# Optimization experiments

Measured on AMD Instinct MI355X. Metric: run time of the kernel, lower is better.

## Reference

```python
import jax, jax.numpy as jnp
import numpy as np

N_NODES = 100000
N_EDGES = 1600000
HIDDEN = 128
N_CLASSES = 40
# torch.rand(1).item() in apply_randalign; fixed here for a deterministic reference
ALPHA = 0.62


def setup_inputs() -> dict:
    key = jax.random.key(0)
    ks = jax.random.split(key, 6)
    inputs = jax.random.normal(ks[0], (N_NODES, HIDDEN), jnp.float32)
    src = jax.random.randint(ks[1], (N_EDGES,), 0, N_NODES, jnp.int32)
    dst = jax.random.randint(ks[2], (N_EDGES,), 0, N_NODES, jnp.int32)
    s = 1.0 / np.sqrt(HIDDEN)
    W1 = jax.random.normal(ks[3], (HIDDEN, HIDDEN), jnp.float32) * s
    W2 = jax.random.normal(ks[4], (HIDDEN, HIDDEN), jnp.float32) * s
    W3 = jax.random.normal(ks[5], (HIDDEN, N_CLASSES), jnp.float32) * s
    return dict(inputs=inputs, src=src, dst=dst,
                W1=W1, b1=jnp.zeros((HIDDEN,), jnp.float32),
                W2=W2, b2=jnp.zeros((HIDDEN,), jnp.float32),
                W3=W3, b3=jnp.zeros((N_CLASSES,), jnp.float32))


def _graph_conv(x, W, b, src, dst):
    # DGL GraphConv, norm='both': D_dst^{-1/2} A D_src^{-1/2} X W + b
    n = x.shape[0]
    ones = jnp.ones(src.shape, x.dtype)
    deg_out = jnp.clip(jax.ops.segment_sum(ones, src, num_segments=n), 1.0)
    deg_in = jnp.clip(jax.ops.segment_sum(ones, dst, num_segments=n), 1.0)
    h = (x @ W) * (deg_out ** -0.5)[:, None]          # row scaling commutes with XW
    agg = jax.ops.segment_sum(h[src], dst, num_segments=n)
    return agg * (deg_in ** -0.5)[:, None] + b


def _randalign(h_prev, h_curr, alpha):
    norm_prev = jnp.linalg.norm(h_prev, axis=1, keepdims=True)
    norm_curr = jnp.linalg.norm(h_curr, axis=1, keepdims=True)
    scaled_prev = h_prev * (norm_curr / norm_prev)
    return alpha * h_curr + (1.0 - alpha) * scaled_prev


def reference(inputs, src, dst, W1, b1, W2, b2, W3, b3):
    # Faithful to source: layers[0] is never applied; loop runs over layers[1..-2].
    h = jax.nn.relu(_graph_conv(inputs, W1, b1, src, dst))      # i = 1
    h_next = jax.nn.relu(_graph_conv(h, W2, b2, src, dst))      # i = 2
    h = _randalign(h, h_next, ALPHA)
    logits = _graph_conv(h, W3, b3, src, dst)                   # final layer
    return logits
```

## Files before the change

### kernel.cpp

```cpp
#include <hip/hip_runtime.h>
#include <hip/hip_bf16.h>

#define HIDDEN 128
#define ALPHA_F 0.62f
#define CAP 64
#define BKT_BITS 9
#define BCAP 10240
#define CSTRIDE 132

typedef __attribute__((ext_vector_type(8))) short bf16x8;
typedef __attribute__((ext_vector_type(4))) float f32x4;

__device__ inline unsigned short f2bf(float f) {
  unsigned u = __float_as_uint(f);
  unsigned r = (u + 0x7fffu + ((u >> 16) & 1u)) >> 16;
  return (unsigned short)r;
}
__device__ inline float bf2f(unsigned short h) {
  return __uint_as_float((unsigned)h << 16);
}

__device__ inline f32x4 mfma_bf16(bf16x8 a, bf16x8 b, f32x4 c) {
  return __builtin_amdgcn_mfma_f32_16x16x32_bf16(a, b, c, 0, 0, 0);
}

template <int CT, bool OUTBF16>
__device__ void gemm_mfma_body(const float* __restrict__ A,
                               const unsigned short* __restrict__ WhT,
                               const unsigned short* __restrict__ WlT,
                               void* __restrict__ outp, int n, int NW, int gi,
                               unsigned* __restrict__ smem) {
  unsigned short* s16 = (unsigned short*)smem;
  const int t = threadIdx.x;
  const int wv = t >> 6, l = t & 63;
  const int lr = l & 15, lg = (l >> 4) & 3;
  const int rb = gi * 128;

  constexpr int WSLOTS = 4 * CT * 64;
  for (int s = t; s < WSLOTS; s += 256) {
    int sl = s & 63;
    int cc = s >> 6;
    int ct = cc % CT, c = cc / CT;
    int col = ct * 16 + (sl & 15);
    int k = c * 32 + ((sl >> 4) & 3) * 8;
    uint4 hv = *(const uint4*)&WhT[(size_t)col * HIDDEN + k];
    uint4 lv = *(const uint4*)&WlT[(size_t)col * HIDDEN + k];
    *(uint4*)&s16[(cc * 2 + 0) * 512 + sl * 8] = hv;
    *(uint4*)&s16[(cc * 2 + 1) * 512 + sl * 8] = lv;
  }

  f32x4 acc[2][CT];
#pragma unroll
  for (int rt = 0; rt < 2; rt++)
#pragma unroll
    for (int ct = 0; ct < CT; ct++)
#pragma unroll
      for (int e = 0; e < 4; e++) acc[rt][ct][e] = 0.f;

  __syncthreads();

  for (int c = 0; c < 4; c++) {
    bf16x8 ah[2], al[2];
#pragma unroll
    for (int rt = 0; rt < 2; rt++) {
      int rr = rb + wv * 32 + rt * 16 + lr;
      if (rr >= n) rr = n - 1;
      const float4* g = (const float4*)(A + (size_t)rr * HIDDEN + c * 32 + lg * 8);
      float4 v0 = g[0], v1 = g[1];
      float f[8] = {v0.x, v0.y, v0.z, v0.w, v1.x, v1.y, v1.z, v1.w};
#pragma unroll
      for (int q = 0; q < 8; q++) {
        unsigned short h = f2bf(f[q]);
        ah[rt][q] = (short)h;
        al[rt][q] = (short)f2bf(f[q] - bf2f(h));
      }
    }
#pragma unroll
    for (int ct = 0; ct < CT; ct++) {
      int cc = c * CT + ct;
      bf16x8 bh = *(const bf16x8*)&s16[(cc * 2 + 0) * 512 + l * 8];
      bf16x8 bl = *(const bf16x8*)&s16[(cc * 2 + 1) * 512 + l * 8];
#pragma unroll
      for (int rt = 0; rt < 2; rt++) {
        acc[rt][ct] = mfma_bf16(ah[rt], bh, acc[rt][ct]);
        acc[rt][ct] = mfma_bf16(al[rt], bh, acc[rt][ct]);
        acc[rt][ct] = mfma_bf16(ah[rt], bl, acc[rt][ct]);
      }
    }
  }

  if (OUTBF16) {
    __syncthreads();
    unsigned short* cr = s16 + wv * (32 * CSTRIDE);
    int lg4 = lg;
#pragma unroll
    for (int rt = 0; rt < 2; rt++)
#pragma unroll
      for (int ct = 0; ct < CT; ct++)
#pragma unroll
        for (int r = 0; r < 4; r++)
          cr[(rt * 16 + lg4 * 4 + r) * CSTRIDE + ct * 16 + lr] = f2bf(acc[rt][ct][r]);
#pragma unroll
    for (int ps = 0; ps < 8; ps++) {
      int row_local = ps * 4 + lg4;
      int orow = rb + wv * 32 + row_local;
      if (orow < n) {
        uint4 v = *(const uint4*)&cr[row_local * CSTRIDE + lr * 8];
        *(uint4*)&((unsigned short*)outp)[(size_t)orow * NW + lr * 8] = v;
      }
    }
  } else {
#pragma unroll
    for (int rt = 0; rt < 2; rt++) {
#pragma unroll
      for (int ct = 0; ct < CT; ct++) {
#pragma unroll
        for (int r = 0; r < 4; r++) {
          int orow = rb + wv * 32 + rt * 16 + lg * 4 + r;
          int ocol = ct * 16 + lr;
          if (orow < n && ocol < NW)
            ((float*)outp)[(size_t)orow * NW + ocol] = acc[rt][ct][r];
        }
      }
    }
  }
}

__global__ __launch_bounds__(256) void partition_kernel(
    const int* __restrict__ src, const int* __restrict__ dst, int E, int nbkt,
    unsigned* __restrict__ gcur1, unsigned* __restrict__ gcur2,
    unsigned* __restrict__ stg1, unsigned short* __restrict__ stg2, int pa_blocks,
    const float* __restrict__ W1, const float* __restrict__ W2, const float* __restrict__ W3,
    unsigned short* __restrict__ W1h, unsigned short* __restrict__ W1l,
    unsigned short* __restrict__ W2h, unsigned short* __restrict__ W2l,
    unsigned short* __restrict__ W3h, unsigned short* __restrict__ W3l, int NC) {
  const int t = threadIdx.x;
  const int bid = blockIdx.x;
  if (bid >= pa_blocks) {
    int r = bid - pa_blocks;
    const float* W = (r == 0) ? W1 : (r == 1) ? W2 : W3;
    unsigned short* Wh = (r == 0) ? W1h : (r == 1) ? W2h : W3h;
    unsigned short* Wl = (r == 0) ? W1l : (r == 1) ? W2l : W3l;
    int ncol = (r == 2) ? 48 : 128;
    int nw   = (r == 2) ? NC : 128;
    for (int idx = t; idx < ncol * HIDDEN; idx += 256) {
      int c = idx >> 7, k = idx & 127;
      float v = (c < nw) ? W[(size_t)k * nw + c] : 0.f;
      unsigned short hi = f2bf(v);
      Wh[idx] = hi;
      Wl[idx] = f2bf(v - bf2f(hi));
    }
    return;
  }
  __shared__ unsigned h1[256], h2[256], b1[256], b2[256];
  h1[t] = 0; h2[t] = 0;
  __syncthreads();
  const int chunk = (E + pa_blocks - 1) / pa_blocks;
  const int e0 = bid * chunk, e1 = min(e0 + chunk, E);
  for (int e = e0 + t; e < e1; e += 256) {
    atomicAdd(&h1[(unsigned)dst[e] >> BKT_BITS], 1u);
    atomicAdd(&h2[(unsigned)src[e] >> BKT_BITS], 1u);
  }
  __syncthreads();
  if (t < nbkt) {
    b1[t] = atomicAdd(&gcur1[t], h1[t]);
    b2[t] = atomicAdd(&gcur2[t], h2[t]);
  }
  h1[t] = 0; h2[t] = 0;
  __syncthreads();
  for (int e = e0 + t; e < e1; e += 256) {
    int s = src[e], d = dst[e];
    unsigned bk1 = (unsigned)d >> BKT_BITS;
    unsigned p1 = b1[bk1] + atomicAdd(&h1[bk1], 1u);
    if (p1 < BCAP) stg1[(size_t)bk1 * BCAP + p1] = ((unsigned)s << BKT_BITS) | ((unsigned)d & 511u);
    unsigned bk2 = (unsigned)s >> BKT_BITS;
    unsigned p2 = b2[bk2] + atomicAdd(&h2[bk2], 1u);
    if (p2 < BCAP) stg2[(size_t)bk2 * BCAP + p2] = (unsigned short)(s & 511);
  }
}

__global__ __launch_bounds__(256) void csr_and_gemm1_kernel(
    const unsigned* __restrict__ gcur1, const unsigned* __restrict__ gcur2,
    const unsigned* __restrict__ stg1, const unsigned short* __restrict__ stg2,
    int* __restrict__ csr, int* __restrict__ deg_in, int* __restrict__ deg_out,
    int n, int nbkt,
    const float* __restrict__ X,
    const unsigned short* __restrict__ W1h, const unsigned short* __restrict__ W1l,
    unsigned short* __restrict__ T1) {
  __shared__ __align__(16) unsigned smem[16384];
  const int bid = blockIdx.x;
  if (bid >= 2 * nbkt) {
    gemm_mfma_body<8, true>(X, W1h, W1l, T1, n, HIDDEN, bid - 2 * nbkt, smem);
    return;
  }
  int* cnt = (int*)smem;
  const int t = threadIdx.x;
  cnt[t] = 0; cnt[t + 256] = 0;
  __syncthreads();
  if (bid < nbkt) {
    const int b = bid;
    const int m = min((int)gcur1[b], BCAP);
    const int node0 = b << BKT_BITS;
    for (int i = t; i < m; i += 256) {
      unsigned val = stg1[(size_t)b * BCAP + i];
      int dl = val & 511;
      int s = (int)(val >> BKT_BITS);
      int pos = atomicAdd(&cnt[dl], 1);
      if (pos < CAP) csr[((size_t)(node0 + dl) << 6) + pos] = s;
    }
    __syncthreads();
    for (int u = t; u < 512; u += 256) {
      int node = node0 + u;
      if (node < n) deg_in[node] = cnt[u];
    }
  } else {
    const int b = bid - nbkt;
    const int m = min((int)gcur2[b], BCAP);
    const int node0 = b << BKT_BITS;
    for (int i = t; i < m; i += 256) {
      atomicAdd(&cnt[stg2[(size_t)b * BCAP + i]], 1);
    }
    __syncthreads();
    for (int u = t; u < 512; u += 256) {
      int node = node0 + u;
      if (node < n) deg_out[node] = cnt[u];
    }
  }
}

__global__ __launch_bounds__(256) void gemm2_kernel(
    const float* __restrict__ A,
    const unsigned short* __restrict__ Wh, const unsigned short* __restrict__ Wl,
    unsigned short* __restrict__ T, int n) {
  __shared__ __align__(16) unsigned smem[16384];
  gemm_mfma_body<8, true>(A, Wh, Wl, T, n, HIDDEN, blockIdx.x, smem);
}

__global__ __launch_bounds__(256) void gemm3_kernel(
    const float* __restrict__ A,
    const unsigned short* __restrict__ Wh, const unsigned short* __restrict__ Wl,
    float* __restrict__ T, int n, int NW) {
  __shared__ __align__(16) unsigned smem[6144];
  gemm_mfma_body<3, false>(A, Wh, Wl, T, n, NW, blockIdx.x, smem);
}

template <bool RA>
__global__ __launch_bounds__(128) void gather_bf16_kernel(
    const unsigned* __restrict__ Tu, const int* __restrict__ csr,
    const int* __restrict__ deg_out, const int* __restrict__ deg_in,
    const float* __restrict__ bias, const float* __restrict__ Hprev,
    float* __restrict__ out, int n) {
  const int w = threadIdx.x >> 6;
  const int lane = threadIdx.x & 63;
  const int v = blockIdx.x * 2 + w;
  if (v >= n) return;
  __shared__ int s_idx[2][64];
  __shared__ float s_w[2][64];
  const int deg = deg_in[v];
  const int m = min(deg, CAP);
  int u0 = (lane < m) ? csr[((size_t)v << 6) + lane] : 0;
  s_idx[w][lane] = u0;
  s_w[w][lane] = (lane < m) ? rsqrtf((float)max(deg_out[u0], 1)) : 0.f;

  float a0 = 0.f, a1 = 0.f, b0 = 0.f, b1 = 0.f, c0 = 0.f, c1 = 0.f, d0 = 0.f, d1 = 0.f;
  int j = 0;
  for (; j + 4 <= m; j += 4) {
    unsigned x0 = Tu[((size_t)s_idx[w][j] << 6) + lane];
    unsigned x1 = Tu[((size_t)s_idx[w][j + 1] << 6) + lane];
    unsigned x2 = Tu[((size_t)s_idx[w][j + 2] << 6) + lane];
    unsigned x3 = Tu[((size_t)s_idx[w][j + 3] << 6) + lane];
    float w0 = s_w[w][j], w1 = s_w[w][j + 1], w2 = s_w[w][j + 2], w3 = s_w[w][j + 3];
    a0 = fmaf(w0, __uint_as_float(x0 << 16), a0);
    a1 = fmaf(w0, __uint_as_float(x0 & 0xffff0000u), a1);
    b0 = fmaf(w1, __uint_as_float(x1 << 16), b0);
    b1 = fmaf(w1, __uint_as_float(x1 & 0xffff0000u), b1);
    c0 = fmaf(w2, __uint_as_float(x2 << 16), c0);
    c1 = fmaf(w2, __uint_as_float(x2 & 0xffff0000u), c1);
    d0 = fmaf(w3, __uint_as_float(x3 << 16), d0);
    d1 = fmaf(w3, __uint_as_float(x3 & 0xffff0000u), d1);
  }
  for (; j < m; j++) {
    unsigned x0 = Tu[((size_t)s_idx[w][j] << 6) + lane];
    float w0 = s_w[w][j];
    a0 = fmaf(w0, __uint_as_float(x0 << 16), a0);
    a1 = fmaf(w0, __uint_as_float(x0 & 0xffff0000u), a1);
  }
  float slo = (a0 + b0) + (c0 + d0);
  float shi = (a1 + b1) + (c1 + d1);
  float din = rsqrtf((float)max(deg, 1));
  float2 bias2 = ((const float2*)bias)[lane];
  float r0 = fmaxf(slo * din + bias2.x, 0.f);
  float r1 = fmaxf(shi * din + bias2.y, 0.f);
  if (RA) {
    float2 p = ((const float2*)(Hprev + (size_t)v * HIDDEN))[lane];
    float sc = r0 * r0 + r1 * r1;
    float sp = p.x * p.x + p.y * p.y;
#pragma unroll
    for (int off = 1; off < 64; off <<= 1) {
      sc += __shfl_xor(sc, off);
      sp += __shfl_xor(sp, off);
    }
    float ratio = sqrtf(sc) / sqrtf(sp);
    r0 = ALPHA_F * r0 + (1.0f - ALPHA_F) * p.x * ratio;
    r1 = ALPHA_F * r1 + (1.0f - ALPHA_F) * p.y * ratio;
  }
  ((float2*)(out + (size_t)v * HIDDEN))[lane] = make_float2(r0, r1);
}

__global__ __launch_bounds__(128) void gather_f32_kernel(
    const float* __restrict__ T3, const int* __restrict__ csr,
    const int* __restrict__ deg_out, const int* __restrict__ deg_in,
    const float* __restrict__ bias, float* __restrict__ out, int n, int NC) {
  const int w = threadIdx.x >> 6;
  const int lane = threadIdx.x & 63;
  const int v = blockIdx.x * 2 + w;
  if (v >= n) return;
  __shared__ int s_idx[2][64];
  __shared__ float s_w[2][64];
  const int deg = deg_in[v];
  const int m = min(deg, CAP);
  int u0 = (lane < m) ? csr[((size_t)v << 6) + lane] : 0;
  s_idx[w][lane] = u0;
  s_w[w][lane] = (lane < m) ? rsqrtf((float)max(deg_out[u0], 1)) : 0.f;

  float a0 = 0.f, a1 = 0.f, a2 = 0.f, a3 = 0.f;
  if (lane < NC) {
    int j = 0;
    for (; j + 4 <= m; j += 4) {
      a0 = fmaf(s_w[w][j],     T3[(size_t)s_idx[w][j] * NC + lane], a0);
      a1 = fmaf(s_w[w][j + 1], T3[(size_t)s_idx[w][j + 1] * NC + lane], a1);
      a2 = fmaf(s_w[w][j + 2], T3[(size_t)s_idx[w][j + 2] * NC + lane], a2);
      a3 = fmaf(s_w[w][j + 3], T3[(size_t)s_idx[w][j + 3] * NC + lane], a3);
    }
    for (; j < m; j++) a0 = fmaf(s_w[w][j], T3[(size_t)s_idx[w][j] * NC + lane], a0);
    float din = rsqrtf((float)max(deg, 1));
    out[(size_t)v * NC + lane] = ((a0 + a1) + (a2 + a3)) * din + bias[lane];
  }
}

extern "C" void kernel_launch(void* const* d_in, const int* in_sizes, int n_in,
                              void* d_out, int out_size, void* d_ws, size_t ws_size,
                              hipStream_t stream) {
  const float* X  = (const float*)d_in[0];
  const int* src  = (const int*)d_in[1];
  const int* dst  = (const int*)d_in[2];
  const float* W1 = (const float*)d_in[3];
  const float* b1 = (const float*)d_in[4];
  const float* W2 = (const float*)d_in[5];
  const float* b2 = (const float*)d_in[6];
  const float* W3 = (const float*)d_in[7];
  const float* b3 = (const float*)d_in[8];
  float* out = (float*)d_out;

  const int n = in_sizes[0] / HIDDEN;
  const int E = in_sizes[1];
  const int NC = in_sizes[8];
  const int nbkt = (n + 511) >> BKT_BITS;

  char* p = (char*)d_ws;
  auto alloc = [&](size_t bytes) {
    char* r = p;
    p += (bytes + 255) & ~(size_t)255;
    return r;
  };
  unsigned* gcur1 = (unsigned*)alloc(512 * 4);
  unsigned* gcur2 = gcur1 + 256;
  int* deg_out    = (int*)alloc((size_t)n * 4);
  int* deg_in     = (int*)alloc((size_t)n * 4);
  int* csr        = (int*)alloc((size_t)n * CAP * 4);
  unsigned short* stg2 = (unsigned short*)alloc((size_t)256 * BCAP * 2);
  unsigned* stg1  = (unsigned*)alloc((size_t)256 * BCAP * 4);
  unsigned short* BufT = (unsigned short*)alloc((size_t)n * HIDDEN * 2);
  float* BufB     = (float*)alloc((size_t)n * HIDDEN * 4);
  unsigned short* W1h = (unsigned short*)alloc(128 * 128 * 2);
  unsigned short* W1l = (unsigned short*)alloc(128 * 128 * 2);
  unsigned short* W2h = (unsigned short*)alloc(128 * 128 * 2);
  unsigned short* W2l = (unsigned short*)alloc(128 * 128 * 2);
  unsigned short* W3h = (unsigned short*)alloc(48 * 128 * 2);
  unsigned short* W3l = (unsigned short*)alloc(48 * 128 * 2);

  hipMemsetAsync(gcur1, 0, 512 * 4, stream);

  const int PA = 256;
  partition_kernel<<<PA + 3, 256, 0, stream>>>(src, dst, E, nbkt, gcur1, gcur2, stg1, stg2, PA,
                                               W1, W2, W3, W1h, W1l, W2h, W2l, W3h, W3l, NC);

  int gb = (n + 127) / 128;
  csr_and_gemm1_kernel<<<2 * nbkt + gb, 256, 0, stream>>>(gcur1, gcur2, stg1, stg2,
                                                          csr, deg_in, deg_out, n, nbkt,
                                                          X, W1h, W1l, BufT);
  int hb = (n + 1) / 2;
  gather_bf16_kernel<false><<<hb, 128, 0, stream>>>((const unsigned*)BufT, csr, deg_out, deg_in, b1, nullptr, BufB, n);
  gemm2_kernel<<<gb, 256, 0, stream>>>(BufB, W2h, W2l, BufT, n);
  gather_bf16_kernel<true><<<hb, 128, 0, stream>>>((const unsigned*)BufT, csr, deg_out, deg_in, b2, BufB, BufB, n);
  gemm3_kernel<<<gb, 256, 0, stream>>>(BufB, W3h, W3l, (float*)BufT, n, NC);
  gather_f32_kernel<<<hb, 128, 0, stream>>>((const float*)BufT, csr, deg_out, deg_in, b3, out, n, NC);
}
```

Baseline: 329.1 us.

## Fuse neighbor gather with following GEMM and store layer-3 features as bf16

Merges each aggregation kernel with the next layer's MFMA GEMM: a 512-thread block gathers 128 node rows into swizzled shared memory as split hi/lo bf16, then multiplies them by the weights, which are read directly from global memory. This removes the fp32 round trip of the hidden activations for layer 2 and of the aligned activations before layer 3, and removes two launches. The layer-3 projection is padded to 64 columns and stored as bf16 instead of fp32, so the final gather reads half as many bytes but with lower precision. Neighbor indices move from shared memory to wave shuffles, and gathering 16 nodes serially per wave may reduce latency hiding.

```diff
diff --git a/kernel.cpp b/kernel.cpp
--- a/kernel.cpp
+++ b/kernel.cpp
@@ -6,7 +6,7 @@
 #define CAP 64
 #define BKT_BITS 9
 #define BCAP 10240
-#define CSTRIDE 132
+#define CSTRIDE 136
 
 typedef __attribute__((ext_vector_type(8))) short bf16x8;
 typedef __attribute__((ext_vector_type(4))) float f32x4;
@@ -24,11 +24,11 @@
   return __builtin_amdgcn_mfma_f32_16x16x32_bf16(a, b, c, 0, 0, 0);
 }
 
-template <int CT, bool OUTBF16>
+template <int CT>
 __device__ void gemm_mfma_body(const float* __restrict__ A,
                                const unsigned short* __restrict__ WhT,
                                const unsigned short* __restrict__ WlT,
-                               void* __restrict__ outp, int n, int NW, int gi,
+                               unsigned short* __restrict__ outp, int n, int NW, int gi,
                                unsigned* __restrict__ smem) {
   unsigned short* s16 = (unsigned short*)smem;
   const int t = threadIdx.x;
@@ -89,39 +89,22 @@
     }
   }
 
-  if (OUTBF16) {
-    __syncthreads();
-    unsigned short* cr = s16 + wv * (32 * CSTRIDE);
-    int lg4 = lg;
-#pragma unroll
-    for (int rt = 0; rt < 2; rt++)
-#pragma unroll
-      for (int ct = 0; ct < CT; ct++)
-#pragma unroll
-        for (int r = 0; r < 4; r++)
-          cr[(rt * 16 + lg4 * 4 + r) * CSTRIDE + ct * 16 + lr] = f2bf(acc[rt][ct][r]);
-#pragma unroll
-    for (int ps = 0; ps < 8; ps++) {
-      int row_local = ps * 4 + lg4;
-      int orow = rb + wv * 32 + row_local;
-      if (orow < n) {
-        uint4 v = *(const uint4*)&cr[row_local * CSTRIDE + lr * 8];
-        *(uint4*)&((unsigned short*)outp)[(size_t)orow * NW + lr * 8] = v;
-      }
-    }
-  } else {
-#pragma unroll
-    for (int rt = 0; rt < 2; rt++) {
-#pragma unroll
-      for (int ct = 0; ct < CT; ct++) {
-#pragma unroll
-        for (int r = 0; r < 4; r++) {
-          int orow = rb + wv * 32 + rt * 16 + lg * 4 + r;
-          int ocol = ct * 16 + lr;
-          if (orow < n && ocol < NW)
-            ((float*)outp)[(size_t)orow * NW + ocol] = acc[rt][ct][r];
-        }
-      }
+  __syncthreads();
+  unsigned short* cr = s16 + wv * (32 * CSTRIDE);
+#pragma unroll
+  for (int rt = 0; rt < 2; rt++)
+#pragma unroll
+    for (int ct = 0; ct < CT; ct++)
+#pragma unroll
+      for (int r = 0; r < 4; r++)
+        cr[(rt * 16 + lg * 4 + r) * CSTRIDE + ct * 16 + lr] = f2bf(acc[rt][ct][r]);
+#pragma unroll
+  for (int ps = 0; ps < 8; ps++) {
+    int row_local = ps * 4 + lg;
+    int orow = rb + wv * 32 + row_local;
+    if (orow < n) {
+      uint4 v = *(const uint4*)&cr[row_local * CSTRIDE + lr * 8];
+      *(uint4*)&outp[(size_t)orow * NW + lr * 8] = v;
     }
   }
 }
@@ -141,7 +124,7 @@
     const float* W = (r == 0) ? W1 : (r == 1) ? W2 : W3;
     unsigned short* Wh = (r == 0) ? W1h : (r == 1) ? W2h : W3h;
     unsigned short* Wl = (r == 0) ? W1l : (r == 1) ? W2l : W3l;
-    int ncol = (r == 2) ? 48 : 128;
+    int ncol = (r == 2) ? 64 : 128;
     int nw   = (r == 2) ? NC : 128;
     for (int idx = t; idx < ncol * HIDDEN; idx += 256) {
       int c = idx >> 7, k = idx & 127;
@@ -190,7 +173,7 @@
   __shared__ __align__(16) unsigned smem[16384];
   const int bid = blockIdx.x;
   if (bid >= 2 * nbkt) {
-    gemm_mfma_body<8, true>(X, W1h, W1l, T1, n, HIDDEN, bid - 2 * nbkt, smem);
+    gemm_mfma_body<8>(X, W1h, W1l, T1, n, HIDDEN, bid - 2 * nbkt, smem);
     return;
   }
   int* cnt = (int*)smem;
@@ -228,113 +211,171 @@
   }
 }
 
-__global__ __launch_bounds__(256) void gemm2_kernel(
-    const float* __restrict__ A,
-    const unsigned short* __restrict__ Wh, const unsigned short* __restrict__ Wl,
-    unsigned short* __restrict__ T, int n) {
-  __shared__ __align__(16) unsigned smem[16384];
-  gemm_mfma_body<8, true>(A, Wh, Wl, T, n, HIDDEN, blockIdx.x, smem);
-}
-
-__global__ __launch_bounds__(256) void gemm3_kernel(
-    const float* __restrict__ A,
-    const unsigned short* __restrict__ Wh, const unsigned short* __restrict__ Wl,
-    float* __restrict__ T, int n, int NW) {
-  __shared__ __align__(16) unsigned smem[6144];
-  gemm_mfma_body<3, false>(A, Wh, Wl, T, n, NW, blockIdx.x, smem);
-}
-
-template <bool RA>
-__global__ __launch_bounds__(128) void gather_bf16_kernel(
+template <int CT, bool RAB>
+__global__ __launch_bounds__(512) void fused_gather_gemm_kernel(
     const unsigned* __restrict__ Tu, const int* __restrict__ csr,
     const int* __restrict__ deg_out, const int* __restrict__ deg_in,
-    const float* __restrict__ bias, const float* __restrict__ Hprev,
-    float* __restrict__ out, int n) {
-  const int w = threadIdx.x >> 6;
-  const int lane = threadIdx.x & 63;
-  const int v = blockIdx.x * 2 + w;
+    const float* __restrict__ bias, float* __restrict__ Hglob,
+    const unsigned short* __restrict__ WhT, const unsigned short* __restrict__ WlT,
+    unsigned short* __restrict__ outT, int n) {
+  __shared__ __align__(16) unsigned short sH[2][128 * 128];
+  const int t = threadIdx.x;
+  const int wv = t >> 6, l = t & 63;
+  const int lr = l & 15, lg = (l >> 4) & 3;
+  const int rb = blockIdx.x * 128;
+
+  for (int nl = 0; nl < 16; nl++) {
+    const int r = wv * 16 + nl;
+    const int v = rb + r;
+    float r0 = 0.f, r1 = 0.f;
+    if (v < n) {
+      const int deg = deg_in[v];
+      const int m = min(deg, CAP);
+      int iu = (l < m) ? csr[((size_t)v << 6) + l] : 0;
+      float wu = (l < m) ? rsqrtf((float)max(deg_out[iu], 1)) : 0.f;
+      float a0 = 0.f, a1 = 0.f, b0 = 0.f, b1 = 0.f, c0 = 0.f, c1 = 0.f, d0 = 0.f, d1 = 0.f;
+      int j = 0;
+      for (; j + 4 <= m; j += 4) {
+        int u0 = __shfl(iu, j), u1 = __shfl(iu, j + 1), u2 = __shfl(iu, j + 2), u3 = __shfl(iu, j + 3);
+        float w0 = __shfl(wu, j), w1 = __shfl(wu, j + 1), w2 = __shfl(wu, j + 2), w3 = __shfl(wu, j + 3);
+        unsigned x0 = Tu[((size_t)u0 << 6) + l];
+        unsigned x1 = Tu[((size_t)u1 << 6) + l];
+        unsigned x2 = Tu[((size_t)u2 << 6) + l];
+        unsigned x3 = Tu[((size_t)u3 << 6) + l];
+        a0 = fmaf(w0, __uint_as_float(x0 << 16), a0);
+        a1 = fmaf(w0, __uint_as_float(x0 & 0xffff0000u), a1);
+        b0 = fmaf(w1, __uint_as_float(x1 << 16), b0);
+        b1 = fmaf(w1, __uint_as_float(x1 & 0xffff0000u), b1);
+        c0 = fmaf(w2, __uint_as_float(x2 << 16), c0);
+        c1 = fmaf(w2, __uint_as_float(x2 & 0xffff0000u), c1);
+        d0 = fmaf(w3, __uint_as_float(x3 << 16), d0);
+        d1 = fmaf(w3, __uint_as_float(x3 & 0xffff0000u), d1);
+      }
+      for (; j < m; j++) {
+        int u0 = __shfl(iu, j);
+        float w0 = __shfl(wu, j);
+        unsigned x0 = Tu[((size_t)u0 << 6) + l];
+        a0 = fmaf(w0, __uint_as_float(x0 << 16), a0);
+        a1 = fmaf(w0, __uint_as_float(x0 & 0xffff0000u), a1);
+      }
+      float slo = (a0 + b0) + (c0 + d0);
+      float shi = (a1 + b1) + (c1 + d1);
+      float din = rsqrtf((float)max(deg, 1));
+      float2 bias2 = ((const float2*)bias)[l];
+      r0 = fmaxf(slo * din + bias2.x, 0.f);
+      r1 = fmaxf(shi * din + bias2.y, 0.f);
+      if (!RAB) {
+        ((float2*)(Hglob + (size_t)v * HIDDEN))[l] = make_float2(r0, r1);
+      } else {
+        float2 pp = ((const float2*)(Hglob + (size_t)v * HIDDEN))[l];
+        float sc = r0 * r0 + r1 * r1;
+        float sp = pp.x * pp.x + pp.y * pp.y;
+#pragma unroll
+        for (int off = 1; off < 64; off <<= 1) {
+          sc += __shfl_xor(sc, off);
+          sp += __shfl_xor(sp, off);
+        }
+        float ratio = sqrtf(sc) / sqrtf(sp);
+        r0 = ALPHA_F * r0 + (1.0f - ALPHA_F) * pp.x * ratio;
+        r1 = ALPHA_F * r1 + (1.0f - ALPHA_F) * pp.y * ratio;
+      }
+    }
+    int off16 = r * 128 + (((l >> 2) ^ (r & 15)) << 3) + ((2 * l) & 7);
+    unsigned short h0 = f2bf(r0), h1v = f2bf(r1);
+    unsigned short q0 = f2bf(r0 - bf2f(h0)), q1 = f2bf(r1 - bf2f(h1v));
+    *(unsigned*)&sH[0][off16] = (unsigned)h0 | ((unsigned)h1v << 16);
+    *(unsigned*)&sH[1][off16] = (unsigned)q0 | ((unsigned)q1 << 16);
+  }
+
+  f32x4 acc[CT];
+#pragma unroll
+  for (int ct = 0; ct < CT; ct++)
+#pragma unroll
+    for (int e = 0; e < 4; e++) acc[ct][e] = 0.f;
+
+  const int ar = wv * 16 + lr;
+  for (int c = 0; c < 4; c++) {
+    int bidx = ((c * 4 + lg) ^ (ar & 15)) << 3;
+    bf16x8 ah = *(const bf16x8*)&sH[0][ar * 128 + bidx];
+    bf16x8 al = *(const bf16x8*)&sH[1][ar * 128 + bidx];
+#pragma unroll
+    for (int ct = 0; ct < CT; ct++) {
+      int col = ct * 16 + lr;
+      bf16x8 bh = *(const bf16x8*)&WhT[(size_t)col * HIDDEN + c * 32 + lg * 8];
+      bf16x8 bl = *(const bf16x8*)&WlT[(size_t)col * HIDDEN + c * 32 + lg * 8];
+      acc[ct] = mfma_bf16(ah, bh, acc[ct]);
+      acc[ct] = mfma_bf16(al, bh, acc[ct]);
+      acc[ct] = mfma_bf16(ah, bl, acc[ct]);
+    }
+  }
+
+  __syncthreads();
+  unsigned short* cr = &sH[0][0] + wv * (16 * CSTRIDE);
+#pragma unroll
+  for (int ct = 0; ct < CT; ct++)
+#pragma unroll
+    for (int r = 0; r < 4; r++)
+      cr[(lg * 4 + r) * CSTRIDE + ct * 16 + lr] = f2bf(acc[ct][r]);
+  constexpr int NW = CT * 16;
+#pragma unroll
+  for (int ps = 0; ps < 4; ps++) {
+    int row_local = ps * 4 + lg;
+    int orow = rb + wv * 16 + row_local;
+    if (orow < n && lr * 8 < NW) {
+      uint4 v = *(const uint4*)&cr[row_local * CSTRIDE + lr * 8];
+      *(uint4*)&outT[(size_t)orow * NW + lr * 8] = v;
+    }
+  }
+}
+
+__global__ __launch_bounds__(256) void gather_final_kernel(
+    const unsigned* __restrict__ Tu3, const int* __restrict__ csr,
+    const int* __restrict__ deg_out, const int* __restrict__ deg_in,
+    const float* __restrict__ bias, float* __restrict__ out, int n, int NC) {
+  const int wv = threadIdx.x >> 6, l = threadIdx.x & 63;
+  const int v = blockIdx.x * 4 + wv;
   if (v >= n) return;
-  __shared__ int s_idx[2][64];
-  __shared__ float s_w[2][64];
   const int deg = deg_in[v];
   const int m = min(deg, CAP);
-  int u0 = (lane < m) ? csr[((size_t)v << 6) + lane] : 0;
-  s_idx[w][lane] = u0;
-  s_w[w][lane] = (lane < m) ? rsqrtf((float)max(deg_out[u0], 1)) : 0.f;
-
+  int iu = (l < m) ? csr[((size_t)v << 6) + l] : 0;
+  float wu = (l < m) ? rsqrtf((float)max(deg_out[iu], 1)) : 0.f;
   float a0 = 0.f, a1 = 0.f, b0 = 0.f, b1 = 0.f, c0 = 0.f, c1 = 0.f, d0 = 0.f, d1 = 0.f;
+  const bool act = (l < 20);
   int j = 0;
   for (; j + 4 <= m; j += 4) {
-    unsigned x0 = Tu[((size_t)s_idx[w][j] << 6) + lane];
-    unsigned x1 = Tu[((size_t)s_idx[w][j + 1] << 6) + lane];
-    unsigned x2 = Tu[((size_t)s_idx[w][j + 2] << 6) + lane];
-    unsigned x3 = Tu[((size_t)s_idx[w][j + 3] << 6) + lane];
-    float w0 = s_w[w][j], w1 = s_w[w][j + 1], w2 = s_w[w][j + 2], w3 = s_w[w][j + 3];
-    a0 = fmaf(w0, __uint_as_float(x0 << 16), a0);
-    a1 = fmaf(w0, __uint_as_float(x0 & 0xffff0000u), a1);
-    b0 = fmaf(w1, __uint_as_float(x1 << 16), b0);
-    b1 = fmaf(w1, __uint_as_float(x1 & 0xffff0000u), b1);
-    c0 = fmaf(w2, __uint_as_float(x2 << 16), c0);
-    c1 = fmaf(w2, __uint_as_float(x2 & 0xffff0000u), c1);
-    d0 = fmaf(w3, __uint_as_float(x3 << 16), d0);
-    d1 = fmaf(w3, __uint_as_float(x3 & 0xffff0000u), d1);
+    int u0 = __shfl(iu, j), u1 = __shfl(iu, j + 1), u2 = __shfl(iu, j + 2), u3 = __shfl(iu, j + 3);
+    float w0 = __shfl(wu, j), w1 = __shfl(wu, j + 1), w2 = __shfl(wu, j + 2), w3 = __shfl(wu, j + 3);
+    if (act) {
+      unsigned x0 = Tu3[((size_t)u0 << 5) + l];
+      unsigned x1 = Tu3[((size_t)u1 << 5) + l];
+      unsigned x2 = Tu3[((size_t)u2 << 5) + l];
+      unsigned x3 = Tu3[((size_t)u3 << 5) + l];
+      a0 = fmaf(w0, __uint_as_float(x0 << 16), a0);
+      a1 = fmaf(w0, __uint_as_float(x0 & 0xffff0000u), a1);
+      b0 = fmaf(w1, __uint_as_float(x1 << 16), b0);
+      b1 = fmaf(w1, __uint_as_float(x1 & 0xffff0000u), b1);
+      c0 = fmaf(w2, __uint_as_float(x2 << 16), c0);
+      c1 = fmaf(w2, __uint_as_float(x2 & 0xffff0000u), c1);
+      d0 = fmaf(w3, __uint_as_float(x3 << 16), d0);
+      d1 = fmaf(w3, __uint_as_float(x3 & 0xffff0000u), d1);
+    }
   }
   for (; j < m; j++) {
-    unsigned x0 = Tu[((size_t)s_idx[w][j] << 6) + lane];
-    float w0 = s_w[w][j];
-    a0 = fmaf(w0, __uint_as_float(x0 << 16), a0);
-    a1 = fmaf(w0, __uint_as_float(x0 & 0xffff0000u), a1);
-  }
-  float slo = (a0 + b0) + (c0 + d0);
-  float shi = (a1 + b1) + (c1 + d1);
-  float din = rsqrtf((float)max(deg, 1));
-  float2 bias2 = ((const float2*)bias)[lane];
-  float r0 = fmaxf(slo * din + bias2.x, 0.f);
-  float r1 = fmaxf(shi * din + bias2.y, 0.f);
-  if (RA) {
-    float2 p = ((const float2*)(Hprev + (size_t)v * HIDDEN))[lane];
-    float sc = r0 * r0 + r1 * r1;
-    float sp = p.x * p.x + p.y * p.y;
-#pragma unroll
-    for (int off = 1; off < 64; off <<= 1) {
-      sc += __shfl_xor(sc, off);
-      sp += __shfl_xor(sp, off);
-    }
-    float ratio = sqrtf(sc) / sqrtf(sp);
-    r0 = ALPHA_F * r0 + (1.0f - ALPHA_F) * p.x * ratio;
-    r1 = ALPHA_F * r1 + (1.0f - ALPHA_F) * p.y * ratio;
-  }
-  ((float2*)(out + (size_t)v * HIDDEN))[lane] = make_float2(r0, r1);
-}
-
-__global__ __launch_bounds__(128) void gather_f32_kernel(
-    const float* __restrict__ T3, const int* __restrict__ csr,
-    const int* __restrict__ deg_out, const int* __restrict__ deg_in,
-    const float* __restrict__ bias, float* __restrict__ out, int n, int NC) {
-  const int w = threadIdx.x >> 6;
-  const int lane = threadIdx.x & 63;
-  const int v = blockIdx.x * 2 + w;
-  if (v >= n) return;
-  __shared__ int s_idx[2][64];
-  __shared__ float s_w[2][64];
-  const int deg = deg_in[v];
-  const int m = min(deg, CAP);
-  int u0 = (lane < m) ? csr[((size_t)v << 6) + lane] : 0;
-  s_idx[w][lane] = u0;
-  s_w[w][lane] = (lane < m) ? rsqrtf((float)max(deg_out[u0], 1)) : 0.f;
-
-  float a0 = 0.f, a1 = 0.f, a2 = 0.f, a3 = 0.f;
-  if (lane < NC) {
-    int j = 0;
-    for (; j + 4 <= m; j += 4) {
-      a0 = fmaf(s_w[w][j],     T3[(size_t)s_idx[w][j] * NC + lane], a0);
-      a1 = fmaf(s_w[w][j + 1], T3[(size_t)s_idx[w][j + 1] * NC + lane], a1);
-      a2 = fmaf(s_w[w][j + 2], T3[(size_t)s_idx[w][j + 2] * NC + lane], a2);
-      a3 = fmaf(s_w[w][j + 3], T3[(size_t)s_idx[w][j + 3] * NC + lane], a3);
-    }
-    for (; j < m; j++) a0 = fmaf(s_w[w][j], T3[(size_t)s_idx[w][j] * NC + lane], a0);
+    int u0 = __shfl(iu, j);
+    float w0 = __shfl(wu, j);
+    if (act) {
+      unsigned x0 = Tu3[((size_t)u0 << 5) + l];
+      a0 = fmaf(w0, __uint_as_float(x0 << 16), a0);
+      a1 = fmaf(w0, __uint_as_float(x0 & 0xffff0000u), a1);
+    }
+  }
+  if (act) {
+    float slo = (a0 + b0) + (c0 + d0);
+    float shi = (a1 + b1) + (c1 + d1);
     float din = rsqrtf((float)max(deg, 1));
-    out[(size_t)v * NC + lane] = ((a0 + a1) + (a2 + a3)) * din + bias[lane];
+    float2 bias2 = ((const float2*)bias)[l];
+    float2 o = make_float2(slo * din + bias2.x, shi * din + bias2.y);
+    *(float2*)(out + (size_t)v * NC + 2 * l) = o;
   }
 }
 
@@ -370,14 +411,15 @@
   int* csr        = (int*)alloc((size_t)n * CAP * 4);
   unsigned short* stg2 = (unsigned short*)alloc((size_t)256 * BCAP * 2);
   unsigned* stg1  = (unsigned*)alloc((size_t)256 * BCAP * 4);
-  unsigned short* BufT = (unsigned short*)alloc((size_t)n * HIDDEN * 2);
+  unsigned short* BufT1 = (unsigned short*)alloc((size_t)n * HIDDEN * 2);
+  unsigned short* BufT2 = (unsigned short*)alloc((size_t)n * HIDDEN * 2);
   float* BufB     = (float*)alloc((size_t)n * HIDDEN * 4);
   unsigned short* W1h = (unsigned short*)alloc(128 * 128 * 2);
   unsigned short* W1l = (unsigned short*)alloc(128 * 128 * 2);
   unsigned short* W2h = (unsigned short*)alloc(128 * 128 * 2);
   unsigned short* W2l = (unsigned short*)alloc(128 * 128 * 2);
-  unsigned short* W3h = (unsigned short*)alloc(48 * 128 * 2);
-  unsigned short* W3l = (unsigned short*)alloc(48 * 128 * 2);
+  unsigned short* W3h = (unsigned short*)alloc(64 * 128 * 2);
+  unsigned short* W3l = (unsigned short*)alloc(64 * 128 * 2);
 
   hipMemsetAsync(gcur1, 0, 512 * 4, stream);
 
@@ -388,11 +430,11 @@
   int gb = (n + 127) / 128;
   csr_and_gemm1_kernel<<<2 * nbkt + gb, 256, 0, stream>>>(gcur1, gcur2, stg1, stg2,
                                                           csr, deg_in, deg_out, n, nbkt,
-                                                          X, W1h, W1l, BufT);
-  int hb = (n + 1) / 2;
-  gather_bf16_kernel<false><<<hb, 128, 0, stream>>>((const unsigned*)BufT, csr, deg_out, deg_in, b1, nullptr, BufB, n);
-  gemm2_kernel<<<gb, 256, 0, stream>>>(BufB, W2h, W2l, BufT, n);
-  gather_bf16_kernel<true><<<hb, 128, 0, stream>>>((const unsigned*)BufT, csr, deg_out, deg_in, b2, BufB, BufB, n);
-  gemm3_kernel<<<gb, 256, 0, stream>>>(BufB, W3h, W3l, (float*)BufT, n, NC);
-  gather_f32_kernel<<<hb, 128, 0, stream>>>((const float*)BufT, csr, deg_out, deg_in, b3, out, n, NC);
-}
+                                                          X, W1h, W1l, BufT1);
+  fused_gather_gemm_kernel<8, false><<<gb, 512, 0, stream>>>(
+      (const unsigned*)BufT1, csr, deg_out, deg_in, b1, BufB, W2h, W2l, BufT2, n);
+  fused_gather_gemm_kernel<4, true><<<gb, 512, 0, stream>>>(
+      (const unsigned*)BufT2, csr, deg_out, deg_in, b2, BufB, W3h, W3l, BufT1, n);
+  gather_final_kernel<<<(n + 3) / 4, 256, 0, stream>>>(
+      (const unsigned*)BufT1, csr, deg_out, deg_in, b3, out, n, NC);
+}
```

Result: slower. 453.0 us (+37.7%).

## Widen gather loads, store layer-3 projection as bf16, process several edges per wave

Applied to the files above, without the earlier changes.

The gather kernels now have each lane load 8 bytes (4 bf16 features), so a single wave handles two neighbors at once (or four in the final layer). Neighbor indices and weights move through wave shuffles instead of shared memory, and the halves are summed with cross-lane reductions. The third GEMM now pads to 64 columns and writes bf16 through the shared-memory staging path, which halves the bytes gathered in the final layer. Blocks grow to 4 waves each. The cost is lower precision in the final-layer intermediate and some extra shuffle work.

```diff
diff --git a/kernel.cpp b/kernel.cpp
--- a/kernel.cpp
+++ b/kernel.cpp
@@ -6,7 +6,7 @@
 #define CAP 64
 #define BKT_BITS 9
 #define BCAP 10240
-#define CSTRIDE 132
+#define CSTRIDE 136
 
 typedef __attribute__((ext_vector_type(8))) short bf16x8;
 typedef __attribute__((ext_vector_type(4))) float f32x4;
@@ -19,16 +19,18 @@
 __device__ inline float bf2f(unsigned short h) {
   return __uint_as_float((unsigned)h << 16);
 }
+__device__ inline float bflo(unsigned x) { return __uint_as_float(x << 16); }
+__device__ inline float bfhi(unsigned x) { return __uint_as_float(x & 0xffff0000u); }
 
 __device__ inline f32x4 mfma_bf16(bf16x8 a, bf16x8 b, f32x4 c) {
   return __builtin_amdgcn_mfma_f32_16x16x32_bf16(a, b, c, 0, 0, 0);
 }
 
-template <int CT, bool OUTBF16>
+template <int CT>
 __device__ void gemm_mfma_body(const float* __restrict__ A,
                                const unsigned short* __restrict__ WhT,
                                const unsigned short* __restrict__ WlT,
-                               void* __restrict__ outp, int n, int NW, int gi,
+                               unsigned short* __restrict__ outp, int n, int NW, int gi,
                                unsigned* __restrict__ smem) {
   unsigned short* s16 = (unsigned short*)smem;
   const int t = threadIdx.x;
@@ -89,39 +91,22 @@
     }
   }
 
-  if (OUTBF16) {
-    __syncthreads();
-    unsigned short* cr = s16 + wv * (32 * CSTRIDE);
-    int lg4 = lg;
-#pragma unroll
-    for (int rt = 0; rt < 2; rt++)
-#pragma unroll
-      for (int ct = 0; ct < CT; ct++)
-#pragma unroll
-        for (int r = 0; r < 4; r++)
-          cr[(rt * 16 + lg4 * 4 + r) * CSTRIDE + ct * 16 + lr] = f2bf(acc[rt][ct][r]);
-#pragma unroll
-    for (int ps = 0; ps < 8; ps++) {
-      int row_local = ps * 4 + lg4;
-      int orow = rb + wv * 32 + row_local;
-      if (orow < n) {
-        uint4 v = *(const uint4*)&cr[row_local * CSTRIDE + lr * 8];
-        *(uint4*)&((unsigned short*)outp)[(size_t)orow * NW + lr * 8] = v;
-      }
-    }
-  } else {
-#pragma unroll
-    for (int rt = 0; rt < 2; rt++) {
-#pragma unroll
-      for (int ct = 0; ct < CT; ct++) {
-#pragma unroll
-        for (int r = 0; r < 4; r++) {
-          int orow = rb + wv * 32 + rt * 16 + lg * 4 + r;
-          int ocol = ct * 16 + lr;
-          if (orow < n && ocol < NW)
-            ((float*)outp)[(size_t)orow * NW + ocol] = acc[rt][ct][r];
-        }
-      }
+  __syncthreads();
+  unsigned short* cr = s16 + wv * (32 * CSTRIDE);
+#pragma unroll
+  for (int rt = 0; rt < 2; rt++)
+#pragma unroll
+    for (int ct = 0; ct < CT; ct++)
+#pragma unroll
+      for (int r = 0; r < 4; r++)
+        cr[(rt * 16 + lg * 4 + r) * CSTRIDE + ct * 16 + lr] = f2bf(acc[rt][ct][r]);
+#pragma unroll
+  for (int ps = 0; ps < 8; ps++) {
+    int row_local = ps * 4 + lg;
+    int orow = rb + wv * 32 + row_local;
+    if (orow < n && lr * 8 < NW) {
+      uint4 v = *(const uint4*)&cr[row_local * CSTRIDE + lr * 8];
+      *(uint4*)&outp[(size_t)orow * NW + lr * 8] = v;
     }
   }
 }
@@ -141,7 +126,7 @@
     const float* W = (r == 0) ? W1 : (r == 1) ? W2 : W3;
     unsigned short* Wh = (r == 0) ? W1h : (r == 1) ? W2h : W3h;
     unsigned short* Wl = (r == 0) ? W1l : (r == 1) ? W2l : W3l;
-    int ncol = (r == 2) ? 48 : 128;
+    int ncol = (r == 2) ? 64 : 128;
     int nw   = (r == 2) ? NC : 128;
     for (int idx = t; idx < ncol * HIDDEN; idx += 256) {
       int c = idx >> 7, k = idx & 127;
@@ -190,7 +175,7 @@
   __shared__ __align__(16) unsigned smem[16384];
   const int bid = blockIdx.x;
   if (bid >= 2 * nbkt) {
-    gemm_mfma_body<8, true>(X, W1h, W1l, T1, n, HIDDEN, bid - 2 * nbkt, smem);
+    gemm_mfma_body<8>(X, W1h, W1l, T1, n, HIDDEN, bid - 2 * nbkt, smem);
     return;
   }
   int* cnt = (int*)smem;
@@ -233,108 +218,119 @@
     const unsigned short* __restrict__ Wh, const unsigned short* __restrict__ Wl,
     unsigned short* __restrict__ T, int n) {
   __shared__ __align__(16) unsigned smem[16384];
-  gemm_mfma_body<8, true>(A, Wh, Wl, T, n, HIDDEN, blockIdx.x, smem);
+  gemm_mfma_body<8>(A, Wh, Wl, T, n, HIDDEN, blockIdx.x, smem);
 }
 
 __global__ __launch_bounds__(256) void gemm3_kernel(
     const float* __restrict__ A,
     const unsigned short* __restrict__ Wh, const unsigned short* __restrict__ Wl,
-    float* __restrict__ T, int n, int NW) {
-  __shared__ __align__(16) unsigned smem[6144];
-  gemm_mfma_body<3, false>(A, Wh, Wl, T, n, NW, blockIdx.x, smem);
+    unsigned short* __restrict__ T, int n) {
+  __shared__ __align__(16) unsigned smem[9000];
+  gemm_mfma_body<4>(A, Wh, Wl, T, n, 64, blockIdx.x, smem);
 }
 
 template <bool RA>
-__global__ __launch_bounds__(128) void gather_bf16_kernel(
+__global__ __launch_bounds__(256) void gather_conv_kernel(
     const unsigned* __restrict__ Tu, const int* __restrict__ csr,
     const int* __restrict__ deg_out, const int* __restrict__ deg_in,
-    const float* __restrict__ bias, const float* __restrict__ Hprev,
-    float* __restrict__ out, int n) {
-  const int w = threadIdx.x >> 6;
-  const int lane = threadIdx.x & 63;
-  const int v = blockIdx.x * 2 + w;
+    const float* __restrict__ bias, float* __restrict__ H, int n) {
+  const int wv = threadIdx.x >> 6, l = threadIdx.x & 63;
+  const int v = blockIdx.x * 4 + wv;
   if (v >= n) return;
-  __shared__ int s_idx[2][64];
-  __shared__ float s_w[2][64];
+  const int half = l >> 5, cg = l & 31;
   const int deg = deg_in[v];
   const int m = min(deg, CAP);
-  int u0 = (lane < m) ? csr[((size_t)v << 6) + lane] : 0;
-  s_idx[w][lane] = u0;
-  s_w[w][lane] = (lane < m) ? rsqrtf((float)max(deg_out[u0], 1)) : 0.f;
-
-  float a0 = 0.f, a1 = 0.f, b0 = 0.f, b1 = 0.f, c0 = 0.f, c1 = 0.f, d0 = 0.f, d1 = 0.f;
+  int iu = (l < m) ? csr[((size_t)v << 6) + l] : 0;
+  float wu = (l < m) ? rsqrtf((float)max(deg_out[iu], 1)) : 0.f;
+
+  const uint2* Tr = (const uint2*)Tu;
+  float a0 = 0.f, a1 = 0.f, a2 = 0.f, a3 = 0.f;
+  float b0 = 0.f, b1 = 0.f, b2 = 0.f, b3 = 0.f;
   int j = 0;
-  for (; j + 4 <= m; j += 4) {
-    unsigned x0 = Tu[((size_t)s_idx[w][j] << 6) + lane];
-    unsigned x1 = Tu[((size_t)s_idx[w][j + 1] << 6) + lane];
-    unsigned x2 = Tu[((size_t)s_idx[w][j + 2] << 6) + lane];
-    unsigned x3 = Tu[((size_t)s_idx[w][j + 3] << 6) + lane];
-    float w0 = s_w[w][j], w1 = s_w[w][j + 1], w2 = s_w[w][j + 2], w3 = s_w[w][j + 3];
-    a0 = fmaf(w0, __uint_as_float(x0 << 16), a0);
-    a1 = fmaf(w0, __uint_as_float(x0 & 0xffff0000u), a1);
-    b0 = fmaf(w1, __uint_as_float(x1 << 16), b0);
-    b1 = fmaf(w1, __uint_as_float(x1 & 0xffff0000u), b1);
-    c0 = fmaf(w2, __uint_as_float(x2 << 16), c0);
-    c1 = fmaf(w2, __uint_as_float(x2 & 0xffff0000u), c1);
-    d0 = fmaf(w3, __uint_as_float(x3 << 16), d0);
-    d1 = fmaf(w3, __uint_as_float(x3 & 0xffff0000u), d1);
-  }
-  for (; j < m; j++) {
-    unsigned x0 = Tu[((size_t)s_idx[w][j] << 6) + lane];
-    float w0 = s_w[w][j];
-    a0 = fmaf(w0, __uint_as_float(x0 << 16), a0);
-    a1 = fmaf(w0, __uint_as_float(x0 & 0xffff0000u), a1);
-  }
-  float slo = (a0 + b0) + (c0 + d0);
-  float shi = (a1 + b1) + (c1 + d1);
+  for (; j + 2 < m; j += 4) {
+    int eA = j + half, eB = j + 2 + half;
+    int uA = __shfl(iu, eA), uB = __shfl(iu, eB);
+    float wA = __shfl(wu, eA), wB = __shfl(wu, eB);
+    uint2 xA = Tr[(size_t)uA * 32 + cg];
+    uint2 xB = Tr[(size_t)uB * 32 + cg];
+    a0 = fmaf(wA, bflo(xA.x), a0); a1 = fmaf(wA, bfhi(xA.x), a1);
+    a2 = fmaf(wA, bflo(xA.y), a2); a3 = fmaf(wA, bfhi(xA.y), a3);
+    b0 = fmaf(wB, bflo(xB.x), b0); b1 = fmaf(wB, bfhi(xB.x), b1);
+    b2 = fmaf(wB, bflo(xB.y), b2); b3 = fmaf(wB, bfhi(xB.y), b3);
+  }
+  for (; j < m; j += 2) {
+    int eA = j + half;
+    int uA = __shfl(iu, eA);
+    float wA = __shfl(wu, eA);
+    uint2 xA = Tr[(size_t)uA * 32 + cg];
+    a0 = fmaf(wA, bflo(xA.x), a0); a1 = fmaf(wA, bfhi(xA.x), a1);
+    a2 = fmaf(wA, bflo(xA.y), a2); a3 = fmaf(wA, bfhi(xA.y), a3);
+  }
+  a0 += b0; a1 += b1; a2 += b2; a3 += b3;
+  a0 += __shfl_xor(a0, 32);
+  a1 += __shfl_xor(a1, 32);
+  a2 += __shfl_xor(a2, 32);
+  a3 += __shfl_xor(a3, 32);
+
   float din = rsqrtf((float)max(deg, 1));
-  float2 bias2 = ((const float2*)bias)[lane];
-  float r0 = fmaxf(slo * din + bias2.x, 0.f);
-  float r1 = fmaxf(shi * din + bias2.y, 0.f);
+  float4 bias4 = ((const float4*)bias)[cg];
+  float r0 = fmaxf(a0 * din + bias4.x, 0.f);
+  float r1 = fmaxf(a1 * din + bias4.y, 0.f);
+  float r2 = fmaxf(a2 * din + bias4.z, 0.f);
+  float r3 = fmaxf(a3 * din + bias4.w, 0.f);
+
   if (RA) {
-    float2 p = ((const float2*)(Hprev + (size_t)v * HIDDEN))[lane];
-    float sc = r0 * r0 + r1 * r1;
-    float sp = p.x * p.x + p.y * p.y;
-#pragma unroll
-    for (int off = 1; off < 64; off <<= 1) {
+    float4 p = ((const float4*)(H + (size_t)v * HIDDEN))[cg];
+    float sc = r0 * r0 + r1 * r1 + r2 * r2 + r3 * r3;
+    float sp = p.x * p.x + p.y * p.y + p.z * p.z + p.w * p.w;
+#pragma unroll
+    for (int off = 1; off < 32; off <<= 1) {
       sc += __shfl_xor(sc, off);
       sp += __shfl_xor(sp, off);
     }
     float ratio = sqrtf(sc) / sqrtf(sp);
     r0 = ALPHA_F * r0 + (1.0f - ALPHA_F) * p.x * ratio;
     r1 = ALPHA_F * r1 + (1.0f - ALPHA_F) * p.y * ratio;
-  }
-  ((float2*)(out + (size_t)v * HIDDEN))[lane] = make_float2(r0, r1);
-}
-
-__global__ __launch_bounds__(128) void gather_f32_kernel(
-    const float* __restrict__ T3, const int* __restrict__ csr,
+    r2 = ALPHA_F * r2 + (1.0f - ALPHA_F) * p.z * ratio;
+    r3 = ALPHA_F * r3 + (1.0f - ALPHA_F) * p.w * ratio;
+  }
+  if (half == 0)
+    ((float4*)(H + (size_t)v * HIDDEN))[cg] = make_float4(r0, r1, r2, r3);
+}
+
+__global__ __launch_bounds__(256) void gather_final_kernel(
+    const unsigned* __restrict__ Tu3, const int* __restrict__ csr,
     const int* __restrict__ deg_out, const int* __restrict__ deg_in,
     const float* __restrict__ bias, float* __restrict__ out, int n, int NC) {
-  const int w = threadIdx.x >> 6;
-  const int lane = threadIdx.x & 63;
-  const int v = blockIdx.x * 2 + w;
+  const int wv = threadIdx.x >> 6, l = threadIdx.x & 63;
+  const int v = blockIdx.x * 4 + wv;
   if (v >= n) return;
-  __shared__ int s_idx[2][64];
-  __shared__ float s_w[2][64];
+  const int q = l >> 4, cg = l & 15;
   const int deg = deg_in[v];
   const int m = min(deg, CAP);
-  int u0 = (lane < m) ? csr[((size_t)v << 6) + lane] : 0;
-  s_idx[w][lane] = u0;
-  s_w[w][lane] = (lane < m) ? rsqrtf((float)max(deg_out[u0], 1)) : 0.f;
-
+  int iu = (l < m) ? csr[((size_t)v << 6) + l] : 0;
+  float wu = (l < m) ? rsqrtf((float)max(deg_out[iu], 1)) : 0.f;
+
+  const uint2* Tr = (const uint2*)Tu3;
   float a0 = 0.f, a1 = 0.f, a2 = 0.f, a3 = 0.f;
-  if (lane < NC) {
-    int j = 0;
-    for (; j + 4 <= m; j += 4) {
-      a0 = fmaf(s_w[w][j],     T3[(size_t)s_idx[w][j] * NC + lane], a0);
-      a1 = fmaf(s_w[w][j + 1], T3[(size_t)s_idx[w][j + 1] * NC + lane], a1);
-      a2 = fmaf(s_w[w][j + 2], T3[(size_t)s_idx[w][j + 2] * NC + lane], a2);
-      a3 = fmaf(s_w[w][j + 3], T3[(size_t)s_idx[w][j + 3] * NC + lane], a3);
-    }
-    for (; j < m; j++) a0 = fmaf(s_w[w][j], T3[(size_t)s_idx[w][j] * NC + lane], a0);
+  for (int j = 0; j < m; j += 4) {
+    int e = j + q;
+    int u = __shfl(iu, e);
+    float w = __shfl(wu, e);
+    uint2 x = Tr[(size_t)u * 16 + cg];
+    a0 = fmaf(w, bflo(x.x), a0); a1 = fmaf(w, bfhi(x.x), a1);
+    a2 = fmaf(w, bflo(x.y), a2); a3 = fmaf(w, bfhi(x.y), a3);
+  }
+  a0 += __shfl_xor(a0, 16); a0 += __shfl_xor(a0, 32);
+  a1 += __shfl_xor(a1, 16); a1 += __shfl_xor(a1, 32);
+  a2 += __shfl_xor(a2, 16); a2 += __shfl_xor(a2, 32);
+  a3 += __shfl_xor(a3, 16); a3 += __shfl_xor(a3, 32);
+  if (l < 10) {
     float din = rsqrtf((float)max(deg, 1));
-    out[(size_t)v * NC + lane] = ((a0 + a1) + (a2 + a3)) * din + bias[lane];
+    float4 bias4 = ((const float4*)bias)[l];
+    float4 o = make_float4(a0 * din + bias4.x, a1 * din + bias4.y,
+                           a2 * din + bias4.z, a3 * din + bias4.w);
+    *(float4*)(out + (size_t)v * NC + 4 * l) = o;
   }
 }
 
@@ -376,8 +372,8 @@
   unsigned short* W1l = (unsigned short*)alloc(128 * 128 * 2);
   unsigned short* W2h = (unsigned short*)alloc(128 * 128 * 2);
   unsigned short* W2l = (unsigned short*)alloc(128 * 128 * 2);
-  unsigned short* W3h = (unsigned short*)alloc(48 * 128 * 2);
-  unsigned short* W3l = (unsigned short*)alloc(48 * 128 * 2);
+  unsigned short* W3h = (unsigned short*)alloc(64 * 128 * 2);
+  unsigned short* W3l = (unsigned short*)alloc(64 * 128 * 2);
 
   hipMemsetAsync(gcur1, 0, 512 * 4, stream);
 
@@ -389,10 +385,13 @@
   csr_and_gemm1_kernel<<<2 * nbkt + gb, 256, 0, stream>>>(gcur1, gcur2, stg1, stg2,
                                                           csr, deg_in, deg_out, n, nbkt,
                                                           X, W1h, W1l, BufT);
-  int hb = (n + 1) / 2;
-  gather_bf16_kernel<false><<<hb, 128, 0, stream>>>((const unsigned*)BufT, csr, deg_out, deg_in, b1, nullptr, BufB, n);
+  int hb = (n + 3) / 4;
+  gather_conv_kernel<false><<<hb, 256, 0, stream>>>(
+      (const unsigned*)BufT, csr, deg_out, deg_in, b1, BufB, n);
   gemm2_kernel<<<gb, 256, 0, stream>>>(BufB, W2h, W2l, BufT, n);
-  gather_bf16_kernel<true><<<hb, 128, 0, stream>>>((const unsigned*)BufT, csr, deg_out, deg_in, b2, BufB, BufB, n);
-  gemm3_kernel<<<gb, 256, 0, stream>>>(BufB, W3h, W3l, (float*)BufT, n, NC);
-  gather_f32_kernel<<<hb, 128, 0, stream>>>((const float*)BufT, csr, deg_out, deg_in, b3, out, n, NC);
-}
+  gather_conv_kernel<true><<<hb, 256, 0, stream>>>(
+      (const unsigned*)BufT, csr, deg_out, deg_in, b2, BufB, n);
+  gemm3_kernel<<<gb, 256, 0, stream>>>(BufB, W3h, W3l, BufT, n);
+  gather_final_kernel<<<hb, 256, 0, stream>>>(
+      (const unsigned*)BufT, csr, deg_out, deg_in, b3, out, n, NC);
+}
```

Measured after the change: 316.1 us. 1.04x faster.
